# Kernel tuning notes

Measured on AMD Instinct MI355X. Metric: run time of the kernel, lower is better.

The kernel has to match this reference:

```python
import jax, jax.numpy as jnp
import numpy as np

NUM_CLASSES = 9
B, H, W = 8, 768, 768


def setup_inputs() -> dict:
    key = jax.random.key(0)
    k1, k2 = jax.random.split(key)
    masks = jax.random.randint(k1, (B, H, W), 0, NUM_CLASSES, dtype=jnp.int32)
    outputs = jax.random.normal(k2, (B, NUM_CLASSES, H, W), dtype=jnp.float32)
    return {"masks": masks, "outputs": outputs}


def reference(masks, outputs):
    b, c, h, w = outputs.shape
    k = NUM_CLASSES
    eye = jnp.eye(k, dtype=outputs.dtype)
    smooth = eye * 0.9 + (1.0 - eye) * (0.1 / 8.0)  # [K, K] smoothed targets

    # Fused segment-mean over all pixels: segment id = batch*K + class label.
    feats = jnp.transpose(outputs, (0, 2, 3, 1)).reshape(b * h * w, c)  # [BHW, C]
    ids = (jnp.arange(b, dtype=jnp.int32)[:, None, None] * k + masks).reshape(-1)
    sums = jax.ops.segment_sum(feats, ids, num_segments=b * k).reshape(b, k, c)
    counts = jax.ops.segment_sum(
        jnp.ones((b * h * w,), outputs.dtype), ids, num_segments=b * k
    ).reshape(b, k)

    # torch.unique(mask)[1:] drops label 0 (background); mask absent classes.
    protos = sums[:, 1:, :] / jnp.maximum(counts[:, 1:, None], 1.0)  # [B, K-1, C]
    present = counts[:, 1:] > 0  # [B, K-1]

    logp = jax.nn.log_softmax(protos, axis=-1)  # [B, K-1, C]
    tgt = smooth[1:]  # [K-1, C] soft targets for classes 1..K-1
    per_proto = -jnp.sum(tgt[None, :, :] * logp, axis=-1)  # [B, K-1]

    n_present = jnp.maximum(jnp.sum(present).astype(outputs.dtype), 1.0)
    loss = jnp.sum(jnp.where(present, per_proto, 0.0)) / n_present
    return loss
```

## Files before the change

kernel.cpp:

```cpp
#include <hip/hip_runtime.h>
#include <hip/hip_bf16.h>
#include <math.h>

#define NB 8
#define NC 9
#define PIXELS (768*768)
#define BLOCK 256
#define PPT 24
#define CHUNK_PX (BLOCK * PPT)
#define NCHUNK (PIXELS / CHUNK_PX)
#define NITER (PPT / 4)

#define SUMS_ELEMS (NB * 8 * NC)
#define WS_FLOATS (SUMS_ELEMS + NB * 8)

__global__ __launch_bounds__(BLOCK)
void accum_kernel(const int* __restrict__ masks,
                  const float* __restrict__ outputs,
                  float* __restrict__ sums,
                  float* __restrict__ counts)
{
    int blk = blockIdx.x;
    int chunk = blk % NCHUNK;
    int b = blk / NCHUNK;
    int t = threadIdx.x;
    int wave = t >> 6;
    int lane = t & 63;

    const int4* __restrict__ m4 =
        (const int4*)(masks + (size_t)b * PIXELS + (size_t)chunk * CHUNK_PX);
    int4 m[NITER];
    #pragma unroll
    for (int i = 0; i < NITER; ++i) m[i] = m4[t + i * BLOCK];

    __shared__ float red[NC][BLOCK / 64][8];
    __shared__ float red_c[BLOCK / 64][8];

    {
        float cnt[8];
        #pragma unroll
        for (int k = 0; k < 8; ++k) cnt[k] = 0.f;
        #pragma unroll
        for (int i = 0; i < NITER; ++i) {
            #pragma unroll
            for (int k = 1; k <= 8; ++k) {
                float a = cnt[k - 1];
                a += (m[i].x == k) ? 1.f : 0.f;
                a += (m[i].y == k) ? 1.f : 0.f;
                a += (m[i].z == k) ? 1.f : 0.f;
                a += (m[i].w == k) ? 1.f : 0.f;
                cnt[k - 1] = a;
            }
        }
        #pragma unroll
        for (int k = 0; k < 8; ++k) {
            float v = cnt[k];
            #pragma unroll
            for (int off = 32; off > 0; off >>= 1) v += __shfl_down(v, off, 64);
            if (lane == 0) red_c[wave][k] = v;
        }
    }

    for (int c = 0; c < NC; ++c) {
        const float4* __restrict__ o4 =
            (const float4*)(outputs + ((size_t)(b * NC + c)) * PIXELS
                            + (size_t)chunk * CHUNK_PX);
        float s[8];
        #pragma unroll
        for (int k = 0; k < 8; ++k) s[k] = 0.f;

        #pragma unroll
        for (int i = 0; i < NITER; ++i) {
            float4 v = o4[t + i * BLOCK];
            #pragma unroll
            for (int k = 1; k <= 8; ++k) {
                float a = s[k - 1];
                a += (m[i].x == k) ? v.x : 0.f;
                a += (m[i].y == k) ? v.y : 0.f;
                a += (m[i].z == k) ? v.z : 0.f;
                a += (m[i].w == k) ? v.w : 0.f;
                s[k - 1] = a;
            }
        }

        #pragma unroll
        for (int k = 0; k < 8; ++k) {
            float v = s[k];
            #pragma unroll
            for (int off = 32; off > 0; off >>= 1) v += __shfl_down(v, off, 64);
            if (lane == 0) red[c][wave][k] = v;
        }
    }

    __syncthreads();

    if (t < NC * 8) {
        int c = t >> 3;
        int k = t & 7;
        float tot = 0.f;
        #pragma unroll
        for (int w = 0; w < BLOCK / 64; ++w) tot += red[c][w][k];
        atomicAdd(&sums[(b * 8 + k) * NC + c], tot);
    } else if (t < NC * 8 + 8) {
        int k = t - NC * 8;
        float tot = 0.f;
        #pragma unroll
        for (int w = 0; w < BLOCK / 64; ++w) tot += red_c[w][k];
        atomicAdd(&counts[b * 8 + k], tot);
    }
}

__global__ __launch_bounds__(64)
void finalize_kernel(const float* __restrict__ sums,
                     const float* __restrict__ counts,
                     float* __restrict__ out)
{
    int t = threadIdx.x;
    int b = t >> 3;
    int cls = t & 7;

    float cntv = counts[b * 8 + cls];
    float denom = fmaxf(cntv, 1.0f);

    float p[NC];
    float mx = -INFINITY;
    #pragma unroll
    for (int c = 0; c < NC; ++c) {
        p[c] = sums[(b * 8 + cls) * NC + c] / denom;
        mx = fmaxf(mx, p[c]);
    }
    float se = 0.f;
    #pragma unroll
    for (int c = 0; c < NC; ++c) se += expf(p[c] - mx);
    float lse = logf(se);

    float per = 0.f;
    #pragma unroll
    for (int c = 0; c < NC; ++c) {
        float tgt = (c == cls + 1) ? 0.9f : 0.0125f;
        per -= tgt * (p[c] - mx - lse);
    }

    bool present = cntv > 0.f;
    float val = present ? per : 0.f;
    float np  = present ? 1.f : 0.f;
    #pragma unroll
    for (int off = 32; off > 0; off >>= 1) {
        val += __shfl_down(val, off, 64);
        np  += __shfl_down(np,  off, 64);
    }
    if (t == 0) out[0] = val / fmaxf(np, 1.f);
}

extern "C" void kernel_launch(void* const* d_in, const int* in_sizes, int n_in,
                              void* d_out, int out_size, void* d_ws, size_t ws_size,
                              hipStream_t stream) {
    const int*   masks   = (const int*)d_in[0];
    const float* outputs = (const float*)d_in[1];
    float* sums   = (float*)d_ws;
    float* counts = sums + SUMS_ELEMS;

    hipMemsetAsync(d_ws, 0, WS_FLOATS * sizeof(float), stream);

    int grid = NB * NCHUNK;
    accum_kernel<<<grid, BLOCK, 0, stream>>>(masks, outputs, sums, counts);
    finalize_kernel<<<1, 64, 0, stream>>>(sums, counts, (float*)d_out);
}
```

Measured before the change: 259.0 us.

## Prefetch next channel, use ballot counts and butterfly transpose reduction

Counts per class are now computed with wave ballot plus popcount instead of per-lane float compares and shuffle reductions. Each channel's output tile is double-buffered in registers, so the load of channel c+1 is issued before channel c is accumulated. The eight per-class shuffle trees are replaced with a transpose-style butterfly that reduces all eight sums using far fewer shuffles. This lowers shuffle/ALU overhead and hides load latency, but the double buffer roughly doubles register pressure, which may reduce occupancy.

```diff
diff --git a/kernel.cpp b/kernel.cpp
--- a/kernel.cpp
+++ b/kernel.cpp
@@ -10,6 +10,7 @@
 #define CHUNK_PX (BLOCK * PPT)
 #define NCHUNK (PIXELS / CHUNK_PX)
 #define NITER (PPT / 4)
+#define NWAVE (BLOCK / 64)
 
 #define SUMS_ELEMS (NB * 8 * NC)
 #define WS_FLOATS (SUMS_ELEMS + NB * 8)
@@ -33,45 +34,58 @@
     #pragma unroll
     for (int i = 0; i < NITER; ++i) m[i] = m4[t + i * BLOCK];
 
-    __shared__ float red[NC][BLOCK / 64][8];
-    __shared__ float red_c[BLOCK / 64][8];
+    __shared__ float red[NC][NWAVE][8];
+    __shared__ float red_c[NWAVE][8];
 
     {
-        float cnt[8];
-        #pragma unroll
-        for (int k = 0; k < 8; ++k) cnt[k] = 0.f;
+        int cnt[8];
+        #pragma unroll
+        for (int k = 0; k < 8; ++k) cnt[k] = 0;
         #pragma unroll
         for (int i = 0; i < NITER; ++i) {
             #pragma unroll
             for (int k = 1; k <= 8; ++k) {
-                float a = cnt[k - 1];
-                a += (m[i].x == k) ? 1.f : 0.f;
-                a += (m[i].y == k) ? 1.f : 0.f;
-                a += (m[i].z == k) ? 1.f : 0.f;
-                a += (m[i].w == k) ? 1.f : 0.f;
-                cnt[k - 1] = a;
+                cnt[k - 1] += __popcll(__ballot(m[i].x == k));
+                cnt[k - 1] += __popcll(__ballot(m[i].y == k));
+                cnt[k - 1] += __popcll(__ballot(m[i].z == k));
+                cnt[k - 1] += __popcll(__ballot(m[i].w == k));
             }
         }
-        #pragma unroll
-        for (int k = 0; k < 8; ++k) {
-            float v = cnt[k];
-            #pragma unroll
-            for (int off = 32; off > 0; off >>= 1) v += __shfl_down(v, off, 64);
-            if (lane == 0) red_c[wave][k] = v;
-        }
-    }
-
+        if (lane == 0) {
+            #pragma unroll
+            for (int k = 0; k < 8; ++k) red_c[wave][k] = (float)cnt[k];
+        }
+    }
+
+    const float* outbase = outputs + (size_t)b * NC * PIXELS + (size_t)chunk * CHUNK_PX;
+
+    float4 buf[NITER];
+    {
+        const float4* o4 = (const float4*)(outbase);
+        #pragma unroll
+        for (int i = 0; i < NITER; ++i) buf[i] = o4[t + i * BLOCK];
+    }
+
+    const int p = lane & 1;
+    const int q = (lane >> 1) & 1;
+    const int r = (lane >> 2) & 1;
+
+    #pragma unroll
     for (int c = 0; c < NC; ++c) {
-        const float4* __restrict__ o4 =
-            (const float4*)(outputs + ((size_t)(b * NC + c)) * PIXELS
-                            + (size_t)chunk * CHUNK_PX);
+        float4 nxt[NITER];
+        if (c < NC - 1) {
+            const float4* o4 = (const float4*)(outbase + (size_t)(c + 1) * PIXELS);
+            #pragma unroll
+            for (int i = 0; i < NITER; ++i) nxt[i] = o4[t + i * BLOCK];
+        }
+
         float s[8];
         #pragma unroll
         for (int k = 0; k < 8; ++k) s[k] = 0.f;
 
         #pragma unroll
         for (int i = 0; i < NITER; ++i) {
-            float4 v = o4[t + i * BLOCK];
+            float4 v = buf[i];
             #pragma unroll
             for (int k = 1; k <= 8; ++k) {
                 float a = s[k - 1];
@@ -83,13 +97,37 @@
             }
         }
 
-        #pragma unroll
-        for (int k = 0; k < 8; ++k) {
-            float v = s[k];
-            #pragma unroll
-            for (int off = 32; off > 0; off >>= 1) v += __shfl_down(v, off, 64);
-            if (lane == 0) red[c][wave][k] = v;
-        }
+        float u[4];
+        #pragma unroll
+        for (int j = 0; j < 4; ++j) {
+            float x = p ? s[j] : s[j + 4];
+            float y = __shfl_xor(x, 1, 64);
+            u[j] = (p ? s[j + 4] : s[j]) + y;
+        }
+        float v2[2];
+        #pragma unroll
+        for (int j = 0; j < 2; ++j) {
+            float x = q ? u[j] : u[j + 2];
+            float y = __shfl_xor(x, 2, 64);
+            v2[j] = (q ? u[j + 2] : u[j]) + y;
+        }
+        float w;
+        {
+            float x = r ? v2[0] : v2[1];
+            float y = __shfl_xor(x, 4, 64);
+            w = (r ? v2[1] : v2[0]) + y;
+        }
+        w += __shfl_xor(w, 8, 64);
+        w += __shfl_xor(w, 16, 64);
+        w += __shfl_xor(w, 32, 64);
+
+        if (lane < 8) {
+            int cls = (p << 2) | (q << 1) | r;
+            red[c][wave][cls] = w;
+        }
+
+        #pragma unroll
+        for (int i = 0; i < NITER; ++i) buf[i] = nxt[i];
     }
 
     __syncthreads();
@@ -99,13 +137,13 @@
         int k = t & 7;
         float tot = 0.f;
         #pragma unroll
-        for (int w = 0; w < BLOCK / 64; ++w) tot += red[c][w][k];
+        for (int w = 0; w < NWAVE; ++w) tot += red[c][w][k];
         atomicAdd(&sums[(b * 8 + k) * NC + c], tot);
     } else if (t < NC * 8 + 8) {
         int k = t - NC * 8;
         float tot = 0.f;
         #pragma unroll
-        for (int w = 0; w < BLOCK / 64; ++w) tot += red_c[w][k];
+        for (int w = 0; w < NWAVE; ++w) tot += red_c[w][k];
         atomicAdd(&counts[b * 8 + k], tot);
     }
 }
```

After: 260.3 us. Within noise of the previous version (+0.5%).
